# Kernel optimization log

Hardware: AMD Instinct MI355X
Metric: run time of the kernel (lower is better)

## Reference

```python
import jax, jax.numpy as jnp
import numpy as np

N_NODES = 100000
N_EDGES = 1600000
D_IN, D_HID, D_OUT = 256, 128, 64


def setup_inputs() -> dict:
    key = jax.random.key(0)
    k = jax.random.split(key, 6)
    x = jax.random.normal(k[0], (N_NODES, D_IN), dtype=jnp.float32)
    edge_index = jax.random.randint(k[1], (2, N_EDGES), 0, N_NODES, dtype=jnp.int64)
    W1 = jax.random.normal(k[2], (D_IN, D_HID), dtype=jnp.float32) / np.sqrt(D_IN)
    b1 = jnp.zeros((D_HID,), dtype=jnp.float32)
    W2 = jax.random.normal(k[3], (D_HID, D_OUT), dtype=jnp.float32) / np.sqrt(D_HID)
    b2 = jnp.zeros((D_OUT,), dtype=jnp.float32)
    return {"x": x, "edge_index": edge_index, "W1": W1, "b1": b1, "W2": W2, "b2": b2}


def gcn_conv(x, W, b, src, dst, n):
    """PyG GCNConv: h = D^-1/2 (A+I) D^-1/2 (x W) + b, symmetric norm with self-loops."""
    h = x @ W                                           # [n, d_out]
    # degree from destination (col) index, +1 for the self-loop edge weight
    deg = jnp.ones((n,), x.dtype).at[dst].add(jnp.float32(1.0))
    dinv = jax.lax.rsqrt(deg)                           # deg >= 1, no inf
    norm = dinv[src] * dinv[dst]                        # [E]
    agg = jax.ops.segment_sum(h[src] * norm[:, None], dst, num_segments=n)
    agg = agg + h * (dinv * dinv)[:, None]              # self-loop contribution
    return agg + b


def reference(x, edge_index, W1, b1, W2, b2):
    src, dst = edge_index[0], edge_index[1]
    n = x.shape[0]
    h = gcn_conv(x, W1, b1, src, dst, n)
    h = jax.nn.relu(h)                                  # dropout is identity in eval mode
    out = gcn_conv(h, W2, b2, src, dst, n)
    return out
```

## Files before the change

### kernel.cpp

```cpp
#include <hip/hip_runtime.h>
#include <stdint.h>

typedef unsigned short u16;
typedef unsigned int u32;
typedef __bf16 bf16x8 __attribute__((ext_vector_type(8)));
typedef float floatx4 __attribute__((ext_vector_type(4)));

static __device__ __forceinline__ float bf2f(u16 u) {
  union { u32 i; float f; } v; v.i = ((u32)u) << 16; return v.f;
}
static __device__ __forceinline__ u16 f2bf(float f) {
  union { float f; u32 i; } v; v.f = f;
  u32 u = v.i;
  return (u16)((u + 0x7fffu + ((u >> 16) & 1u)) >> 16);
}

static __device__ __forceinline__ void gload_lds16(const void* g, void* l) {
  __builtin_amdgcn_global_load_lds(
      (const __attribute__((address_space(1))) void*)g,
      (__attribute__((address_space(3))) void*)l, 16, 0, 0);
}

__global__ void k_edgemode(const int* __restrict__ ei, int* __restrict__ flag) {
  int t = threadIdx.x;
  int v = ei[2 * t + 1];
  unsigned long long b = __ballot(v == 0);
  if (t == 0) *flag = (b == ~0ull) ? 1 : 0;
}

static __device__ __forceinline__ int edge_src(const int* ei, int E, int i, int m64) {
  return m64 ? ei[2 * (size_t)i] : ei[i];
}
static __device__ __forceinline__ int edge_dst(const int* ei, int E, int i, int m64) {
  return m64 ? ei[2 * (size_t)E + 2 * (size_t)i] : ei[(size_t)E + i];
}

__global__ void k_transpose(const float* __restrict__ W1, const float* __restrict__ W2,
                            u16* __restrict__ Wt1, u16* __restrict__ Wt2) {
  int i = blockIdx.x * 256 + threadIdx.x;
  if (i < 256 * 128) {
    int k = i >> 7, c = i & 127;
    Wt1[c * 256 + k] = f2bf(W1[i]);
  } else {
    int j = i - 256 * 128;
    if (j < 128 * 64) {
      int k = j >> 6, c = j & 63;
      Wt2[c * 128 + k] = f2bf(W2[j]);
    }
  }
}

#define CHUNK 2048

__global__ void k_count(const int* __restrict__ ei, int E, const int* __restrict__ flag,
                        int* __restrict__ bucket_cnt, int NB) {
  __shared__ int h[1024];
  const int t = threadIdx.x;
  for (int i = t; i < 1024; i += 256) h[i] = 0;
  __syncthreads();
  const int c0 = blockIdx.x * CHUNK;
  const int cnt = min(CHUNK, E - c0);
  const int m64 = *flag;
  for (int i = t; i < cnt; i += 256)
    atomicAdd(&h[edge_dst(ei, E, c0 + i, m64) >> 7], 1);
  __syncthreads();
  for (int i = t; i < NB; i += 256)
    if (h[i]) atomicAdd(&bucket_cnt[i], h[i]);
}

__global__ void k_bscan(const int* __restrict__ bucket_cnt, int* __restrict__ bucket_base,
                        int* __restrict__ bucket_cursor, int NB,
                        int* __restrict__ row_ptr, int n, int E) {
  __shared__ int ts[256];
  const int t = threadIdx.x;
  const int b4 = t * 4;
  int a0 = (b4 + 0 < NB) ? bucket_cnt[b4 + 0] : 0;
  int a1 = (b4 + 1 < NB) ? bucket_cnt[b4 + 1] : 0;
  int a2 = (b4 + 2 < NB) ? bucket_cnt[b4 + 2] : 0;
  int a3 = (b4 + 3 < NB) ? bucket_cnt[b4 + 3] : 0;
  int p1 = a0, p2 = p1 + a1, p3 = p2 + a2, tsum = p3 + a3;
  ts[t] = tsum;
  __syncthreads();
  for (int off = 1; off < 256; off <<= 1) {
    int x = (t >= off) ? ts[t - off] : 0;
    __syncthreads();
    ts[t] += x;
    __syncthreads();
  }
  int ex0 = ts[t] - tsum;
  int e[4] = {ex0, ex0 + p1, ex0 + p2, ex0 + p3};
#pragma unroll
  for (int j = 0; j < 4; ++j) {
    int i = b4 + j;
    if (i < NB) { bucket_base[i] = e[j]; bucket_cursor[i] = e[j]; }
  }
  if (t == 0) row_ptr[n] = E + n;
}

__global__ void k_place(const int* __restrict__ ei, int E, const int* __restrict__ flag,
                        int* __restrict__ bucket_cursor, uint2* __restrict__ pairs, int NB) {
  __shared__ int h[1024];
  __shared__ int ex[1024];
  __shared__ int cur[1024];
  __shared__ int ts[256];
  __shared__ uint2 stage[CHUNK];
  const int t = threadIdx.x;
  const int c0 = blockIdx.x * CHUNK;
  const int cnt = min(CHUNK, E - c0);
  const int m64 = *flag;

  for (int i = t; i < 1024; i += 256) h[i] = 0;
  __syncthreads();

  int es[8], ed[8];
#pragma unroll
  for (int j = 0; j < 8; ++j) {
    int i = t + j * 256;
    es[j] = 0; ed[j] = -1;
    if (i < cnt) {
      es[j] = edge_src(ei, E, c0 + i, m64);
      ed[j] = edge_dst(ei, E, c0 + i, m64);
      atomicAdd(&h[ed[j] >> 7], 1);
    }
  }
  __syncthreads();

  const int b4 = t * 4;
  int a0 = h[b4], a1 = h[b4 + 1], a2 = h[b4 + 2], a3 = h[b4 + 3];
  int p1 = a0, p2 = p1 + a1, p3 = p2 + a2, tsum = p3 + a3;
  ts[t] = tsum;
  __syncthreads();
  for (int off = 1; off < 256; off <<= 1) {
    int x = (t >= off) ? ts[t - off] : 0;
    __syncthreads();
    ts[t] += x;
    __syncthreads();
  }
  int ex0 = ts[t] - tsum;
  ex[b4] = ex0;       cur[b4] = ex0;
  ex[b4 + 1] = ex0 + p1; cur[b4 + 1] = ex0 + p1;
  ex[b4 + 2] = ex0 + p2; cur[b4 + 2] = ex0 + p2;
  ex[b4 + 3] = ex0 + p3; cur[b4 + 3] = ex0 + p3;
  __syncthreads();

#pragma unroll
  for (int j = 0; j < 8; ++j) {
    if (ed[j] >= 0) {
      int b = ed[j] >> 7;
      int pos = atomicAdd(&cur[b], 1);
      stage[pos] = make_uint2((u32)es[j], (u32)ed[j]);
    }
  }
  __syncthreads();
  for (int i = t; i < NB; i += 256) {
    int c = h[i];
    if (c > 0) h[i] = atomicAdd(&bucket_cursor[i], c);
  }
  __syncthreads();

  for (int i = t; i < cnt; i += 256) {
    uint2 p = stage[i];
    int b = (int)(p.y >> 7);
    pairs[h[b] + (i - ex[b])] = p;
  }
}

#define BMAX 3072
__global__ void k_csr(const uint2* __restrict__ pairs, const int* __restrict__ bucket_cnt,
                      const int* __restrict__ bucket_base, int* __restrict__ row_ptr,
                      float* __restrict__ dinv, int* __restrict__ srcs, int n) {
  __shared__ int h[128], cur[128];
  __shared__ int lsrc[BMAX];
  const int b = blockIdx.x;
  const int t = threadIdx.x;
  const int cnt = bucket_cnt[b];
  const int base = bucket_base[b];
  const int nbase = base + b * 128;

  if (t < 128) h[t] = 0;
  __syncthreads();
  for (int i = t; i < cnt; i += 256)
    atomicAdd(&h[pairs[base + i].y & 127], 1);
  __syncthreads();

  __shared__ int sc[128];
  int v = 0;
  if (t < 128) { v = h[t]; sc[t] = v; }
  __syncthreads();
  for (int off = 1; off < 128; off <<= 1) {
    int x = 0;
    if (t < 128 && t >= off) x = sc[t - off];
    __syncthreads();
    if (t < 128) sc[t] += x;
    __syncthreads();
  }
  if (t < 128) {
    int excl = sc[t] - v;
    cur[t] = excl + t + 1;
    int node = b * 128 + t;
    if (node < n) {
      row_ptr[node] = nbase + excl + t;
      dinv[node] = rsqrtf(1.0f + (float)v);
      int sp = excl + t;
      if (sp < BMAX) lsrc[sp] = node;
      else srcs[nbase + sp] = node;
    }
  }
  __syncthreads();

  for (int i = t; i < cnt; i += 256) {
    uint2 p = pairs[base + i];
    int pos = atomicAdd(&cur[p.y & 127], 1);
    if (pos < BMAX) lsrc[pos] = (int)p.x;
    else srcs[nbase + pos] = (int)p.x;
  }
  __syncthreads();
  const int lim = min(cnt + 128, BMAX);
  for (int i = t; i < lim; i += 256) srcs[nbase + i] = lsrc[i];
}

template<int N, int K, int CHK, bool A_FP32>
__launch_bounds__(256, 4)
__global__ void k_gemm(const void* __restrict__ Ap, const u16* __restrict__ Wt,
                       const float* __restrict__ dinv, u16* __restrict__ G, int M)
{
  constexpr int ESZ  = A_FP32 ? 4 : 2;
  constexpr int BPR  = K * ESZ;
  constexpr int BPRC = CHK * ESZ;
  constexpr int RPI  = 1024 / BPRC;
  constexpr int NISS = 64 / RPI;
  constexpr int STRIDE = 1024 + 16;
  constexpr int NCH  = K / CHK;
  constexpr int KSC  = CHK / 32;
  constexpr int IPW  = NISS / 4;
  constexpr int LPR  = BPRC / 16;
  constexpr int SWM  = 8 / RPI;
  constexpr int NT   = N / 32;
  __shared__ char lds[2 * NISS * STRIDE];
  const int t = threadIdx.x;
  const int wave = t >> 6, lane = t & 63;
  const int row0 = blockIdx.x * 64;
  const int wr = wave >> 1, wc = wave & 1;
  const int lm = lane & 15, lq = lane >> 4;

  const int ril  = lane / LPR;
  const int scol = ((lane % LPR) ^ (ril * SWM)) * 16;

  auto stage = [&](int kc) {
    char* buf = lds + (size_t)(kc & 1) * (NISS * STRIDE);
    const size_t kb = (size_t)kc * BPRC;
#pragma unroll
    for (int i = 0; i < IPW; ++i) {
      const int g = wave * IPW + i;
      int r0 = row0 + g * RPI;
      if (r0 < M) {
        if (r0 > M - RPI) r0 = M - RPI;
        gload_lds16((const char*)Ap + (size_t)(r0 + ril) * BPR + kb + scol,
                    buf + g * STRIDE);
      }
    }
  };

  floatx4 acc[2][NT];
#pragma unroll
  for (int i = 0; i < 2; ++i)
#pragma unroll
    for (int j = 0; j < NT; ++j) acc[i][j] = (floatx4)(0.0f);

  const int arow = wr * 32 + lm;
  const u16* pb = Wt + (size_t)(wc * (N / 2) + lm) * K + lq * 8;

  stage(0);

#pragma unroll
  for (int c = 0; c < NCH; ++c) {
    bf16x8 breg[KSC][NT];
#pragma unroll
    for (int ksl = 0; ksl < KSC; ++ksl)
#pragma unroll
      for (int nt = 0; nt < NT; ++nt)
        breg[ksl][nt] = *(const bf16x8*)(pb + (size_t)nt * 16 * K + (c * KSC + ksl) * 32);

    if (c + 1 < NCH) {
      stage(c + 1);
      asm volatile("s_waitcnt vmcnt(%0)" :: "i"(IPW) : "memory");
    } else {
      asm volatile("s_waitcnt vmcnt(0)" ::: "memory");
    }
    __builtin_amdgcn_sched_barrier(0);
    __builtin_amdgcn_s_barrier();
    __builtin_amdgcn_sched_barrier(0);

    const char* buf = lds + (size_t)(c & 1) * (NISS * STRIDE);
#pragma unroll
    for (int ksl = 0; ksl < KSC; ++ksl) {
      bf16x8 a[2];
#pragma unroll
      for (int mt = 0; mt < 2; ++mt) {
        const int r = arow + mt * 16;
        const int cb = (ksl * 32 + lq * 8) * ESZ;
        const char* p = buf + (r / RPI) * STRIDE + (r % RPI) * BPRC
                        + (cb ^ ((r % RPI) * SWM * 16));
        if constexpr (A_FP32) {
          float4 f0 = *(const float4*)p;
          float4 f1 = *(const float4*)(p + 16);
          bf16x8 av;
          av[0] = (__bf16)f0.x; av[1] = (__bf16)f0.y; av[2] = (__bf16)f0.z; av[3] = (__bf16)f0.w;
          av[4] = (__bf16)f1.x; av[5] = (__bf16)f1.y; av[6] = (__bf16)f1.z; av[7] = (__bf16)f1.w;
          a[mt] = av;
        } else {
          a[mt] = *(const bf16x8*)p;
        }
      }
#pragma unroll
      for (int nt = 0; nt < NT; ++nt) {
        acc[0][nt] = __builtin_amdgcn_mfma_f32_16x16x32_bf16(a[0], breg[ksl][nt], acc[0][nt], 0, 0, 0);
        acc[1][nt] = __builtin_amdgcn_mfma_f32_16x16x32_bf16(a[1], breg[ksl][nt], acc[1][nt], 0, 0, 0);
      }
    }
    __builtin_amdgcn_sched_barrier(0);
    __builtin_amdgcn_s_barrier();
  }

  const int crow0 = row0 + wr * 32 + lq * 4;
#pragma unroll
  for (int mt = 0; mt < 2; ++mt) {
#pragma unroll
    for (int nt = 0; nt < NT; ++nt) {
      const int gc = wc * (N / 2) + nt * 16 + lm;
#pragma unroll
      for (int r = 0; r < 4; ++r) {
        const int gr = crow0 + mt * 16 + r;
        if (gr < M) G[(size_t)gr * N + gc] = f2bf(acc[mt][nt][r] * dinv[gr]);
      }
    }
  }
}

template<int F, bool RELU, bool OUT_BF16, int NPW>
__launch_bounds__(256, 4)
__global__ void k_agg(const u16* __restrict__ g, const int* __restrict__ row_ptr,
                      const int* __restrict__ srcs, const float* __restrict__ dinv,
                      const float* __restrict__ bias, void* __restrict__ outp, int n)
{
  const int wid = blockIdx.x * 4 + (threadIdx.x >> 6);
  const int n0 = wid * NPW;
  if (n0 >= n) return;
  const int n1 = min(n0 + NPW, n);
  const int lane = threadIdx.x & 63;
  constexpr int VPL = F / 64;
  const int col = lane * VPL;
  const float b0 = bias[col];
  const float b1 = (VPL == 2) ? bias[col + (VPL - 1)] : 0.f;

  int e    = __builtin_amdgcn_readfirstlane(row_ptr[n0]);
  int eEnd = __builtin_amdgcn_readfirstlane(row_ptr[n1]);
  int cur  = n0;
  int nb   = __builtin_amdgcn_readfirstlane(row_ptr[n0 + 1]);
  float dv = dinv[n0];
  float a0 = 0.f, a1 = 0.f;

  auto fin = [&]() {
    float o0 = dv * a0 + b0;
    if (RELU) o0 = fmaxf(o0, 0.f);
    if constexpr (VPL == 2) {
      float o1 = dv * a1 + b1;
      if (RELU) o1 = fmaxf(o1, 0.f);
      if constexpr (OUT_BF16) {
        u32 pk = (u32)f2bf(o0) | ((u32)f2bf(o1) << 16);
        *(u32*)((u16*)outp + (size_t)cur * F + col) = pk;
      } else {
        *(float2*)((float*)outp + (size_t)cur * F + col) = make_float2(o0, o1);
      }
    } else {
      if constexpr (OUT_BF16) ((u16*)outp)[(size_t)cur * F + col] = f2bf(o0);
      else                    ((float*)outp)[(size_t)cur * F + col] = o0;
    }
    ++cur;
    a0 = 0.f; a1 = 0.f;
    if (cur < n) {
      dv = dinv[cur];
      nb = __builtin_amdgcn_readfirstlane(row_ptr[cur + 1]);
    }
  };

  auto issue = [&](int eb, u32* gv) {
    const int* sp = srcs + eb;
#pragma unroll
    for (int j = 0; j < 8; ++j) {
      const int s = sp[j];
      if constexpr (VPL == 2)
        gv[j] = *(const u32*)(g + (size_t)s * F + col);
      else
        gv[j] = (u32)g[(size_t)s * F + col];
    }
  };

  auto consume = [&](int eb, const u32* gv) {
#pragma unroll
    for (int j = 0; j < 8; ++j) {
      if (eb + j == nb) fin();
      if constexpr (VPL == 2) {
        a0 += bf2f((u16)gv[j]);
        a1 += bf2f((u16)(gv[j] >> 16));
      } else {
        a0 += bf2f((u16)gv[j]);
      }
    }
  };

  u32 gvA[8], gvB[8];
  const int rem = (eEnd - e) >> 3;
  if (rem >= 1) issue(e, gvA);
  if (rem >= 2) issue(e + 8, gvB);
  int i = 0;
  for (; i + 2 < rem; i += 2) {
    consume(e + i * 8, gvA);
    issue(e + (i + 2) * 8, gvA);
    consume(e + (i + 1) * 8, gvB);
    if (i + 3 < rem) issue(e + (i + 3) * 8, gvB);
  }
  if (i < rem) { consume(e + i * 8, gvA); ++i; }
  if (i < rem) { consume(e + i * 8, gvB); ++i; }

  for (int et = e + rem * 8; et < eEnd; ++et) {
    const int s = srcs[et];
    u32 gvt;
    if constexpr (VPL == 2) gvt = *(const u32*)(g + (size_t)s * F + col);
    else                    gvt = (u32)g[(size_t)s * F + col];
    if (et == nb) fin();
    if constexpr (VPL == 2) { a0 += bf2f((u16)gvt); a1 += bf2f((u16)(gvt >> 16)); }
    else                    a0 += bf2f((u16)gvt);
  }
  fin();
}

extern "C" void kernel_launch(void* const* d_in, const int* in_sizes, int n_in,
                              void* d_out, int out_size, void* d_ws, size_t ws_size,
                              hipStream_t stream)
{
  const float* x  = (const float*)d_in[0];
  const int*   ei = (const int*)d_in[1];
  const float* W1 = (const float*)d_in[2];
  const float* b1 = (const float*)d_in[3];
  const float* W2 = (const float*)d_in[4];
  const float* b2 = (const float*)d_in[5];

  const int n = in_sizes[0] / 256;
  const int E = in_sizes[1] / 2;
  const int NB = (n + 127) >> 7;

  char* ws = (char*)d_ws;
  size_t off = 0;
  auto alloc = [&](size_t bytes) -> void* {
    void* p = ws + off;
    off = (off + bytes + 255) & ~(size_t)255;
    return p;
  };
  int*   row_ptr = (int*)alloc((size_t)(n + 1) * 4);
  int*   bcnt    = (int*)alloc(1024 * 4);
  int*   bbase   = (int*)alloc(1024 * 4);
  int*   bcur    = (int*)alloc(1024 * 4);
  int*   eflag   = (int*)alloc(256);
  float* dinv    = (float*)alloc((size_t)n * 4);
  u16*   Wt1     = (u16*)alloc(256 * 128 * 2);
  u16*   Wt2     = (u16*)alloc(128 * 64 * 2);
  uint2* pairs   = (uint2*)alloc((size_t)E * 8);
  int*   srcs    = (int*)alloc((size_t)(E + n + 512) * 4);
  u16*   g1      = (u16*)alloc((size_t)n * 128 * 2);
  u16*   y1      = (u16*)alloc((size_t)n * 128 * 2);
  u16*   g2      = (u16*)alloc((size_t)n * 64 * 2);
  (void)ws_size; (void)n_in; (void)out_size;

  const int TB = 256;
  const int nbC = (E + CHUNK - 1) / CHUNK;

  hipMemsetAsync(bcnt, 0, 1024 * 4, stream);
  k_edgemode<<<1, 64, 0, stream>>>(ei, eflag);
  k_transpose<<<(256 * 128 + 128 * 64 + TB - 1) / TB, TB, 0, stream>>>(W1, W2, Wt1, Wt2);
  k_count<<<nbC, TB, 0, stream>>>(ei, E, eflag, bcnt, NB);
  k_bscan<<<1, TB, 0, stream>>>(bcnt, bbase, bcur, NB, row_ptr, n, E);
  k_place<<<nbC, TB, 0, stream>>>(ei, E, eflag, bcur, pairs, NB);
  k_csr<<<NB, TB, 0, stream>>>(pairs, bcnt, bbase, row_ptr, dinv, srcs, n);

  constexpr int NPW = 8;
  const int nwaves = (n + NPW - 1) / NPW;
  const int aggGrid = (nwaves + 3) / 4;

  k_gemm<128, 256, 64, true><<<(n + 63) / 64, 256, 0, stream>>>(x, Wt1, dinv, g1, n);
  k_agg<128, true, true, NPW><<<aggGrid, 256, 0, stream>>>(g1, row_ptr, srcs, dinv, b1, y1, n);
  k_gemm<64, 128, 64, false><<<(n + 63) / 64, 256, 0, stream>>>(y1, Wt2, dinv, g2, n);
  k_agg<64, false, false, NPW><<<aggGrid, 256, 0, stream>>>(g2, row_ptr, srcs, dinv, b2, d_out, n);
}
```

Measured before the change: 375.0 us.

## Shrink GEMM tiles to 32 rows with 2 waves and K-chunk 32

Restructures the GEMM kernel to use 32-row blocks with 128 threads (two waves split across output columns) and a fixed K-chunk of 32, removing the inner K sub-loop. Smaller tiles yield more blocks and less LDS per block, aiming at higher occupancy and better latency hiding on the bandwidth-bound GEMMs. The row bound check in staging is dropped, relying on clamping. The aggregation kernel's launch bounds are also raised to request more waves per SIMD, which may force register spills.

```diff
diff --git a/kernel.cpp b/kernel.cpp
--- a/kernel.cpp
+++ b/kernel.cpp
@@ -219,45 +219,42 @@
   for (int i = t; i < lim; i += 256) srcs[nbase + i] = lsrc[i];
 }
 
-template<int N, int K, int CHK, bool A_FP32>
-__launch_bounds__(256, 4)
+template<int N, int K, bool A_FP32>
+__launch_bounds__(128, 6)
 __global__ void k_gemm(const void* __restrict__ Ap, const u16* __restrict__ Wt,
                        const float* __restrict__ dinv, u16* __restrict__ G, int M)
 {
   constexpr int ESZ  = A_FP32 ? 4 : 2;
-  constexpr int BPR  = K * ESZ;
+  constexpr int CHK  = 32;
+  constexpr int NCH  = K / CHK;
   constexpr int BPRC = CHK * ESZ;
   constexpr int RPI  = 1024 / BPRC;
-  constexpr int NISS = 64 / RPI;
+  constexpr int NISS = 32 / RPI;
+  constexpr int IPW  = NISS / 2;
   constexpr int STRIDE = 1024 + 16;
-  constexpr int NCH  = K / CHK;
-  constexpr int KSC  = CHK / 32;
-  constexpr int IPW  = NISS / 4;
+  constexpr int SWM  = 8 / RPI;
   constexpr int LPR  = BPRC / 16;
-  constexpr int SWM  = 8 / RPI;
   constexpr int NT   = N / 32;
+  constexpr int BPR  = K * ESZ;
   __shared__ char lds[2 * NISS * STRIDE];
   const int t = threadIdx.x;
-  const int wave = t >> 6, lane = t & 63;
-  const int row0 = blockIdx.x * 64;
-  const int wr = wave >> 1, wc = wave & 1;
+  const int wc = t >> 6, lane = t & 63;
+  const int row0 = blockIdx.x * 32;
   const int lm = lane & 15, lq = lane >> 4;
 
   const int ril  = lane / LPR;
   const int scol = ((lane % LPR) ^ (ril * SWM)) * 16;
 
-  auto stage = [&](int kc) {
-    char* buf = lds + (size_t)(kc & 1) * (NISS * STRIDE);
-    const size_t kb = (size_t)kc * BPRC;
+  auto stage = [&](int c) {
+    char* buf = lds + (c & 1) * (NISS * STRIDE);
+    const size_t kb = (size_t)c * BPRC;
 #pragma unroll
     for (int i = 0; i < IPW; ++i) {
-      const int g = wave * IPW + i;
+      const int g = wc * IPW + i;
       int r0 = row0 + g * RPI;
-      if (r0 < M) {
-        if (r0 > M - RPI) r0 = M - RPI;
-        gload_lds16((const char*)Ap + (size_t)(r0 + ril) * BPR + kb + scol,
-                    buf + g * STRIDE);
-      }
+      if (r0 > M - RPI) r0 = M - RPI;
+      gload_lds16((const char*)Ap + (size_t)(r0 + ril) * BPR + kb + scol,
+                  buf + g * STRIDE);
     }
   };
 
@@ -267,19 +264,16 @@
 #pragma unroll
     for (int j = 0; j < NT; ++j) acc[i][j] = (floatx4)(0.0f);
 
-  const int arow = wr * 32 + lm;
   const u16* pb = Wt + (size_t)(wc * (N / 2) + lm) * K + lq * 8;
 
   stage(0);
 
 #pragma unroll
   for (int c = 0; c < NCH; ++c) {
-    bf16x8 breg[KSC][NT];
-#pragma unroll
-    for (int ksl = 0; ksl < KSC; ++ksl)
-#pragma unroll
-      for (int nt = 0; nt < NT; ++nt)
-        breg[ksl][nt] = *(const bf16x8*)(pb + (size_t)nt * 16 * K + (c * KSC + ksl) * 32);
+    bf16x8 breg[NT];
+#pragma unroll
+    for (int nt = 0; nt < NT; ++nt)
+      breg[nt] = *(const bf16x8*)(pb + (size_t)nt * 16 * K + c * CHK);
 
     if (c + 1 < NCH) {
       stage(c + 1);
@@ -291,38 +285,34 @@
     __builtin_amdgcn_s_barrier();
     __builtin_amdgcn_sched_barrier(0);
 
-    const char* buf = lds + (size_t)(c & 1) * (NISS * STRIDE);
-#pragma unroll
-    for (int ksl = 0; ksl < KSC; ++ksl) {
-      bf16x8 a[2];
-#pragma unroll
-      for (int mt = 0; mt < 2; ++mt) {
-        const int r = arow + mt * 16;
-        const int cb = (ksl * 32 + lq * 8) * ESZ;
-        const char* p = buf + (r / RPI) * STRIDE + (r % RPI) * BPRC
-                        + (cb ^ ((r % RPI) * SWM * 16));
-        if constexpr (A_FP32) {
-          float4 f0 = *(const float4*)p;
-          float4 f1 = *(const float4*)(p + 16);
-          bf16x8 av;
-          av[0] = (__bf16)f0.x; av[1] = (__bf16)f0.y; av[2] = (__bf16)f0.z; av[3] = (__bf16)f0.w;
-          av[4] = (__bf16)f1.x; av[5] = (__bf16)f1.y; av[6] = (__bf16)f1.z; av[7] = (__bf16)f1.w;
-          a[mt] = av;
-        } else {
-          a[mt] = *(const bf16x8*)p;
-        }
+    const char* buf = lds + (c & 1) * (NISS * STRIDE);
+    bf16x8 a[2];
+#pragma unroll
+    for (int mt = 0; mt < 2; ++mt) {
+      const int r = mt * 16 + lm;
+      const char* p = buf + (r / RPI) * STRIDE + (r % RPI) * BPRC;
+      const int k0 = (r % RPI) * SWM;
+      if constexpr (A_FP32) {
+        float4 f0 = *(const float4*)(p + (((2 * lq)     ^ k0) * 16));
+        float4 f1 = *(const float4*)(p + (((2 * lq + 1) ^ k0) * 16));
+        bf16x8 av;
+        av[0] = (__bf16)f0.x; av[1] = (__bf16)f0.y; av[2] = (__bf16)f0.z; av[3] = (__bf16)f0.w;
+        av[4] = (__bf16)f1.x; av[5] = (__bf16)f1.y; av[6] = (__bf16)f1.z; av[7] = (__bf16)f1.w;
+        a[mt] = av;
+      } else {
+        a[mt] = *(const bf16x8*)(p + ((lq ^ k0) * 16));
       }
-#pragma unroll
-      for (int nt = 0; nt < NT; ++nt) {
-        acc[0][nt] = __builtin_amdgcn_mfma_f32_16x16x32_bf16(a[0], breg[ksl][nt], acc[0][nt], 0, 0, 0);
-        acc[1][nt] = __builtin_amdgcn_mfma_f32_16x16x32_bf16(a[1], breg[ksl][nt], acc[1][nt], 0, 0, 0);
-      }
+    }
+#pragma unroll
+    for (int nt = 0; nt < NT; ++nt) {
+      acc[0][nt] = __builtin_amdgcn_mfma_f32_16x16x32_bf16(a[0], breg[nt], acc[0][nt], 0, 0, 0);
+      acc[1][nt] = __builtin_amdgcn_mfma_f32_16x16x32_bf16(a[1], breg[nt], acc[1][nt], 0, 0, 0);
     }
     __builtin_amdgcn_sched_barrier(0);
     __builtin_amdgcn_s_barrier();
   }
 
-  const int crow0 = row0 + wr * 32 + lq * 4;
+  const int crow0 = row0 + lq * 4;
 #pragma unroll
   for (int mt = 0; mt < 2; ++mt) {
 #pragma unroll
@@ -338,7 +328,7 @@
 }
 
 template<int F, bool RELU, bool OUT_BF16, int NPW>
-__launch_bounds__(256, 4)
+__launch_bounds__(256, 8)
 __global__ void k_agg(const u16* __restrict__ g, const int* __restrict__ row_ptr,
                       const int* __restrict__ srcs, const float* __restrict__ dinv,
                       const float* __restrict__ bias, void* __restrict__ outp, int n)
@@ -487,8 +477,8 @@
   const int nwaves = (n + NPW - 1) / NPW;
   const int aggGrid = (nwaves + 3) / 4;
 
-  k_gemm<128, 256, 64, true><<<(n + 63) / 64, 256, 0, stream>>>(x, Wt1, dinv, g1, n);
+  k_gemm<128, 256, true><<<(n + 31) / 32, 128, 0, stream>>>(x, Wt1, dinv, g1, n);
   k_agg<128, true, true, NPW><<<aggGrid, 256, 0, stream>>>(g1, row_ptr, srcs, dinv, b1, y1, n);
-  k_gemm<64, 128, 64, false><<<(n + 63) / 64, 256, 0, stream>>>(y1, Wt2, dinv, g2, n);
+  k_gemm<64, 128, false><<<(n + 31) / 32, 128, 0, stream>>>(y1, Wt2, dinv, g2, n);
   k_agg<64, false, false, NPW><<<aggGrid, 256, 0, stream>>>(g2, row_ptr, srcs, dinv, b2, d_out, n);
 }
```

After: 384.0 us. 2.4% more time.
